# Performance work log

Measured on AMD Instinct MI355X. Metric: run time of the kernel, lower is better.

Reference implementation:

```python
import jax, jax.numpy as jnp
import numpy as np

B, L, D = 4, 1024, 1024
N, H = 16, 64
FFW = 4096
LYR = 6
PDIM = 768            # 3 * 16^2
POS_EMB = 64
POOL_K = 4
EPS = 1e-6
BASE = 10000.0
GRID = 32             # 32x32 patch grid


def rms_norm(x, scale=None, eps=EPS):
    v = jnp.mean(jnp.square(x.astype(jnp.float32)), axis=-1, keepdims=True)
    y = (x.astype(jnp.float32) * jax.lax.rsqrt(v + eps)).astype(x.dtype)
    return y * scale if scale is not None else y


def _rope_half(x, pos, base):
    # x: [B, L, N, Hh]; pos: [B, L] int coords
    Hh = x.shape[-1]
    inv = 1.0 / (base ** (jnp.arange(Hh // 2, dtype=jnp.float32) / (Hh // 2)))
    ang = pos.astype(jnp.float32)[..., None] * inv          # [B, L, Hh/2]
    cos = jnp.cos(ang)[:, :, None, :]
    sin = jnp.sin(ang)[:, :, None, :]
    x1, x2 = jnp.split(x, 2, axis=-1)
    return jnp.concatenate([x1 * cos - x2 * sin, x2 * cos + x1 * sin], axis=-1)


def apply_2d_rope(x, px, py, base):
    # first half of head_dim rotated by x-coord, second half by y-coord
    xa, xb = jnp.split(x, 2, axis=-1)
    return jnp.concatenate([_rope_half(xa, px, base), _rope_half(xb, py, base)], axis=-1)


def setup_inputs() -> dict:
    key = jax.random.key(0)
    ks = jax.random.split(key, 12)
    pixel_values = jax.random.uniform(ks[0], (B, L, PDIM), dtype=jnp.float32)
    gx = jnp.arange(L, dtype=jnp.int32) % GRID
    gy = jnp.arange(L, dtype=jnp.int32) // GRID
    position_ids = jnp.broadcast_to(jnp.stack([gx, gy], -1), (B, L, 2))
    s = 0.02
    Win = jax.random.normal(ks[1], (PDIM, D), jnp.float32) * s
    pos_table = jax.random.normal(ks[2], (2, POS_EMB, D), jnp.float32) * s
    Wq = jax.random.normal(ks[3], (LYR, D, N * H), jnp.float32) * s
    Wk = jax.random.normal(ks[4], (LYR, D, N * H), jnp.float32) * s
    Wv = jax.random.normal(ks[5], (LYR, D, N * H), jnp.float32) * s
    Wo = jax.random.normal(ks[6], (LYR, N * H, D), jnp.float32) * s
    Wg = jax.random.normal(ks[7], (LYR, D, FFW), jnp.float32) * s
    Wu = jax.random.normal(ks[8], (LYR, D, FFW), jnp.float32) * s
    Wd = jax.random.normal(ks[9], (LYR, FFW, D), jnp.float32) * s
    qn = jnp.ones((LYR, H), jnp.float32)
    kn = jnp.ones((LYR, H), jnp.float32)
    pre_attn = jnp.ones((LYR, D), jnp.float32)
    post_attn = jnp.ones((LYR, D), jnp.float32)
    pre_ffw = jnp.ones((LYR, D), jnp.float32)
    post_ffw = jnp.ones((LYR, D), jnp.float32)
    return dict(pixel_values=pixel_values, position_ids=position_ids, Win=Win,
                pos_table=pos_table, Wq=Wq, Wk=Wk, Wv=Wv, Wo=Wo, qn=qn, kn=kn,
                pre_attn=pre_attn, post_attn=post_attn, pre_ffw=pre_ffw,
                post_ffw=post_ffw, Wg=Wg, Wu=Wu, Wd=Wd)


def _encoder(pixel_values, position_ids, Win, pos_table, Wq, Wk, Wv, Wo, qn, kn,
             pre_attn, post_attn, pre_ffw, post_ffw, Wg, Wu, Wd):
    padding = jnp.all(position_ids == -1, axis=-1)          # [B, L] True = pad
    valid = ~padding
    big_neg = jnp.finfo(jnp.float32).min
    amask = jnp.where((valid[:, :, None] & valid[:, None, :])[:, None], 0.0, big_neg)  # [B,1,L,L]

    px = position_ids[:, :, 0]
    py = position_ids[:, :, 1]
    clamped = jnp.maximum(position_ids, 0)

    # patch embed
    pix = 2.0 * (pixel_values - 0.5)
    x = pix @ Win
    pos_emb = pos_table[0][clamped[..., 0]] + pos_table[1][clamped[..., 1]]
    x = x + jnp.where(padding[..., None], 0.0, pos_emb)

    for i in range(LYR):
        # attention
        res = x
        h = rms_norm(x, pre_attn[i])
        q = (h @ Wq[i]).reshape(B, L, N, H)
        k = (h @ Wk[i]).reshape(B, L, N, H)
        v = (h @ Wv[i]).reshape(B, L, N, H)
        q = rms_norm(q, qn[i])
        k = rms_norm(k, kn[i])
        v = rms_norm(v)                                     # with_scale=False
        q = apply_2d_rope(q, px, py, BASE)
        k = apply_2d_rope(k, px, py, BASE)
        scores = jnp.einsum('bqnh,bknh->bnqk', q, k) + amask  # no 1/sqrt(H), matches source
        w = jax.nn.softmax(scores.astype(jnp.float32), axis=-1).astype(v.dtype)
        o = jnp.einsum('bnqk,bknh->bqnh', w, v).reshape(B, L, N * H) @ Wo[i]
        x = res + rms_norm(o, post_attn[i])
        # GeGLU MLP
        res = x
        h = rms_norm(x, pre_ffw[i])
        m = (jax.nn.gelu(h @ Wg[i], approximate=True) * (h @ Wu[i])) @ Wd[i]
        x = res + rms_norm(m, post_ffw[i])

    # pooler: 4x4 position-based average pooling
    out_len = L // (POOL_K ** 2)
    kk = int((L / out_len) ** 0.5)
    x = jnp.where(padding[..., None], 0.0, x)
    max_x = jnp.max(clamped[..., 0], axis=-1, keepdims=True) + 1   # [B,1]
    kidx = clamped // kk
    kidx = kidx[..., 0] + (max_x // kk) * kidx[..., 1]             # [B, L]
    weights = jax.nn.one_hot(kidx, out_len, dtype=jnp.float32) / (kk * kk)
    pooled = jnp.einsum('blo,bld->bod', weights, x.astype(jnp.float32))
    mask = jnp.any(weights != 0, axis=1)                           # [B, out_len]
    pooled = pooled.astype(x.dtype) * jnp.sqrt(jnp.float32(D))
    pooled = jnp.where(mask[..., None], pooled, 0.0)               # jit-safe stand-in for hidden[mask]
    return pooled, mask


def reference(pixel_values, position_ids, Win, pos_table, Wq, Wk, Wv, Wo, qn, kn,
              pre_attn, post_attn, pre_ffw, post_ffw, Wg, Wu, Wd):
    return _encoder(pixel_values, position_ids, Win, pos_table, Wq, Wk, Wv, Wo,
                    qn, kn, pre_attn, post_attn, pre_ffw, post_ffw, Wg, Wu, Wd)
```

## Files before the change

kernel.cpp:

```cpp
#include <hip/hip_runtime.h>
#include <stdint.h>

typedef unsigned short ushort_t;
using frag8 = __attribute__((ext_vector_type(8))) short;
using f32x4 = __attribute__((ext_vector_type(4))) float;

static __device__ __forceinline__ unsigned short f2bf(float f) {
  union { float f; unsigned u; } v; v.f = f;
  unsigned r = v.u + 0x7fffu + ((v.u >> 16) & 1u);
  return (unsigned short)(r >> 16);
}
static __device__ __forceinline__ float bf2f(unsigned short b) {
  union { unsigned u; float f; } v; v.u = ((unsigned)b) << 16; return v.f;
}
static __device__ __forceinline__ void splitf(float v, ushort_t& h, ushort_t& m) {
  h = f2bf(v);
  m = f2bf(v - bf2f(h));
}

__global__ __launch_bounds__(256) void k_splitpix(const float* __restrict__ pix,
                                                  ushort_t* __restrict__ oh,
                                                  ushort_t* __restrict__ om, int n4) {
  int i = blockIdx.x * 256 + threadIdx.x;
  if (i >= n4) return;
// ... 32 lines not shown
  int n = tid >> 2;
  int kc = (tid & 3) << 4;
  ushort_t oh[16], om[16];
#pragma unroll
  for (int j = 0; j < 16; ++j) splitf(ts[kc + j][n], oh[j], om[j]);
  ushort_t* ph = th + (size_t)(n0 + n) * K + k0 + kc;
  ushort_t* pm = tm + (size_t)(n0 + n) * K + k0 + kc;
  *(uint4*)(ph) = *(uint4*)(oh);
  *(uint4*)(ph + 8) = *(uint4*)(oh + 8);
  *(uint4*)(pm) = *(uint4*)(om);
  *(uint4*)(pm + 8) = *(uint4*)(om + 8);
}

__global__ __launch_bounds__(256) void k_posemb(const int* __restrict__ pos,
                                                const float* __restrict__ ptab,
                                                float* __restrict__ x) {
  int row = blockIdx.x, tid = threadIdx.x;
  int p0 = pos[(size_t)row * 2], p1 = pos[(size_t)row * 2 + 1];
  bool pad = (p0 == -1) && (p1 == -1);
  int px = p0 > 0 ? p0 : 0, py = p1 > 0 ? p1 : 0;
  float4 a = ((const float4*)(ptab + (size_t)px * 1024))[tid];
  float4 b = ((const float4*)(ptab + 65536 + (size_t)py * 1024))[tid];
  float4 o;
  o.x = pad ? 0.f : a.x + b.x;
  o.y = pad ? 0.f : a.y + b.y;
  o.z = pad ? 0.f : a.z + b.z;
  o.w = pad ? 0.f : a.w + b.w;
  ((float4*)(x + (size_t)row * 1024))[tid] = o;
}

__global__ __launch_bounds__(256) void k_rmsnorm_s(const float* __restrict__ x,
                                                   const float* __restrict__ scale,
                                                   ushort_t* __restrict__ oh,
                                                   ushort_t* __restrict__ om) {
  __shared__ float wsum[4];
  int row = blockIdx.x, tid = threadIdx.x;
  float4 v = ((const float4*)(x + (size_t)row * 1024))[tid];
  float ss = v.x * v.x + v.y * v.y + v.z * v.z + v.w * v.w;
  for (int m = 1; m < 64; m <<= 1) ss += __shfl_xor(ss, m);
  if ((tid & 63) == 0) wsum[tid >> 6] = ss;
  __syncthreads();
  float tot = wsum[0] + wsum[1] + wsum[2] + wsum[3];
  float r = rsqrtf(tot * (1.f / 1024.f) + 1e-6f);
  float4 sc = ((const float4*)scale)[tid];
  ushort4 h, m;
  splitf(v.x * r * sc.x, h.x, m.x);
  splitf(v.y * r * sc.y, h.y, m.y);
  splitf(v.z * r * sc.z, h.z, m.z);
  splitf(v.w * r * sc.w, h.w, m.w);
  ((ushort4*)(oh + (size_t)row * 1024))[tid] = h;
  ((ushort4*)(om + (size_t)row * 1024))[tid] = m;
}

__global__ __launch_bounds__(256) void k_addrms32(float* __restrict__ x,
                                                  const float* __restrict__ t1,
                                                  const float* __restrict__ t2,
                                                  const float* __restrict__ scale) {
  __shared__ float wsum[4];
  int row = blockIdx.x, tid = threadIdx.x;
  float4 v = ((const float4*)(t1 + (size_t)row * 1024))[tid];
  float4 v2 = ((const float4*)(t2 + (size_t)row * 1024))[tid];
  v.x += v2.x; v.y += v2.y; v.z += v2.z; v.w += v2.w;
  float ss = v.x * v.x + v.y * v.y + v.z * v.z + v.w * v.w;
  for (int m = 1; m < 64; m <<= 1) ss += __shfl_xor(ss, m);
  if ((tid & 63) == 0) wsum[tid >> 6] = ss;
  __syncthreads();
  float tot = wsum[0] + wsum[1] + wsum[2] + wsum[3];
  float r = rsqrtf(tot * (1.f / 1024.f) + 1e-6f);
  float4 sc = ((const float4*)scale)[tid];
  float4 xv = ((const float4*)(x + (size_t)row * 1024))[tid];
  xv.x += v.x * r * sc.x;
  xv.y += v.y * r * sc.y;
  xv.z += v.z * r * sc.z;
  xv.w += v.w * r * sc.w;
  ((float4*)(x + (size_t)row * 1024))[tid] = xv;
}

#define SWZ_COL(r, c) (((c) ^ (((r) >> 3) & 3)) << 3)

__global__ __launch_bounds__(256) void k_qkv(const ushort_t* __restrict__ Ah,
                                             const ushort_t* __restrict__ Am,
                                             const ushort_t* __restrict__ WT_h,
                                             const ushort_t* __restrict__ WT_m,
                                             const float* __restrict__ qn,
                                             const float* __restrict__ kn,
                                             const int* __restrict__ pos,
                                             ushort_t* __restrict__ qh, ushort_t* __restrict__ qm,
                                             ushort_t* __restrict__ kh, ushort_t* __restrict__ km,
                                             ushort_t* __restrict__ vh, ushort_t* __restrict__ vm) {
  __shared__ __align__(16) ushort_t Ash[128][40];
  __shared__ __align__(16) ushort_t Asl[128][40];
  __shared__ __align__(16) ushort_t Bsh[128][40];
  __shared__ __align__(16) ushort_t Bsl[128][40];
  const int tid = threadIdx.x;
  const int bid = blockIdx.x;
  const int xcd = bid & 7, lo = bid >> 3;
  const int ntl = lo % 3, mt = lo / 3;
  const int nt = xcd * 3 + ntl;
  const int mat = nt >> 3;
  const int n0 = (nt & 7) << 7;
  const int m0 = mt << 7;
  const ushort_t* Bh = WT_h + (size_t)mat * 1048576;
  const ushort_t* Bm = WT_m + (size_t)mat * 1048576;

  const int lane = tid & 63;
  const int wm = ((tid >> 7) & 1) * 64;
  const int wn = ((tid >> 6) & 1) * 64;
  const int l15 = lane & 15, lg = lane >> 4;
  const int srow = tid >> 1, scol = (tid & 1) << 4;
  const int cb = (tid & 1) << 1;
  const int wc0 = SWZ_COL(srow, cb), wc1 = SWZ_COL(srow, cb + 1);
  f32x4 acc[4][4] = {};

  for (int k0 = 0; k0 < 1024; k0 += 32) {
    const ushort_t* gah = Ah + (size_t)(m0 + srow) * 1024 + k0 + scol;
    const ushort_t* gam = Am + (size_t)(m0 + srow) * 1024 + k0 + scol;
    const ushort_t* gbh = Bh + (size_t)(n0 + srow) * 1024 + k0 + scol;
    const ushort_t* gbm = Bm + (size_t)(n0 + srow) * 1024 + k0 + scol;
    uint4 a0 = *(const uint4*)gah, a1 = *(const uint4*)(gah + 8);
    uint4 a2 = *(const uint4*)gam, a3 = *(const uint4*)(gam + 8);
    uint4 b0 = *(const uint4*)gbh, b1 = *(const uint4*)(gbh + 8);
    uint4 b2 = *(const uint4*)gbm, b3 = *(const uint4*)(gbm + 8);
    *(uint4*)(&Ash[srow][wc0]) = a0;
    *(uint4*)(&Ash[srow][wc1]) = a1;
    *(uint4*)(&Asl[srow][wc0]) = a2;
    *(uint4*)(&Asl[srow][wc1]) = a3;
    *(uint4*)(&Bsh[srow][wc0]) = b0;
    *(uint4*)(&Bsh[srow][wc1]) = b1;
    *(uint4*)(&Bsl[srow][wc0]) = b2;
    *(uint4*)(&Bsl[srow][wc1]) = b3;
    __syncthreads();
    frag8 ah[4], al[4], bh[4], bl[4];
#pragma unroll
    for (int i = 0; i < 4; ++i) {
      int rA = wm + i * 16 + l15, rB = wn + i * 16 + l15;
      int cA = SWZ_COL(rA, lg), cB = SWZ_COL(rB, lg);
      ah[i] = *(const frag8*)(&Ash[rA][cA]);
      al[i] = *(const frag8*)(&Asl[rA][cA]);
      bh[i] = *(const frag8*)(&Bsh[rB][cB]);
      bl[i] = *(const frag8*)(&Bsl[rB][cB]);
    }
#pragma unroll
    for (int mi = 0; mi < 4; ++mi)
#pragma unroll
      for (int ni = 0; ni < 4; ++ni) {
        acc[mi][ni] = __builtin_amdgcn_mfma_f32_16x16x32_bf16(ah[mi], bh[ni], acc[mi][ni], 0, 0, 0);
        acc[mi][ni] = __builtin_amdgcn_mfma_f32_16x16x32_bf16(ah[mi], bl[ni], acc[mi][ni], 0, 0, 0);
        acc[mi][ni] = __builtin_amdgcn_mfma_f32_16x16x32_bf16(al[mi], bh[ni], acc[mi][ni], 0, 0, 0);
      }
    __syncthreads();
  }

  const float* scale = (mat == 0) ? qn : (mat == 1 ? kn : nullptr);
  ushort_t* outh = (mat == 0) ? qh : (mat == 1 ? kh : vh);
  ushort_t* outm = (mat == 0) ? qm : (mat == 1 ? km : vm);
  const float inv = powf(10000.f, -(float)l15 * (1.f / 16.f));
#pragma unroll
  for (int mi = 0; mi < 4; ++mi) {
#pragma unroll
    for (int rr = 0; rr < 4; ++rr) {
      float ss = 0.f;
#pragma unroll
      for (int ni = 0; ni < 4; ++ni) { float v = acc[mi][ni][rr]; ss += v * v; }
      ss += __shfl_xor(ss, 1);
      ss += __shfl_xor(ss, 2);
      ss += __shfl_xor(ss, 4);
      ss += __shfl_xor(ss, 8);
      float rs = rsqrtf(ss * (1.f / 64.f) + 1e-6f);
      int row = m0 + wm + mi * 16 + (lg << 2) + rr;
      float nv[4];
#pragma unroll
      for (int ni = 0; ni < 4; ++ni) {
        float sc = scale ? scale[ni * 16 + l15] : 1.f;
        nv[ni] = acc[mi][ni][rr] * rs * sc;
      }
      if (mat < 2) {
        int p0 = pos[(size_t)row * 2], p1 = pos[(size_t)row * 2 + 1];
        p0 = p0 > 0 ? p0 : 0;
        p1 = p1 > 0 ? p1 : 0;
        float a0 = (float)p0 * inv, a1 = (float)p1 * inv;
        float c0 = cosf(a0), s0 = sinf(a0);
        float c1 = cosf(a1), s1 = sinf(a1);
        float t0 = nv[0] * c0 - nv[1] * s0;
        float t1 = nv[1] * c0 + nv[0] * s0;
        float t2 = nv[2] * c1 - nv[3] * s1;
        float t3 = nv[3] * c1 + nv[2] * s1;
        nv[0] = t0; nv[1] = t1; nv[2] = t2; nv[3] = t3;
      }
#pragma unroll
      for (int ni = 0; ni < 4; ++ni) {
        ushort_t h, m;
        splitf(nv[ni], h, m);
        size_t idx = (size_t)row * 1024 + n0 + wn + ni * 16 + l15;
        outh[idx] = h;
        outm[idx] = m;
      }
    }
  }
}

__global__ __launch_bounds__(256) void k_ffw_up(const ushort_t* __restrict__ Ah,
                                                const ushort_t* __restrict__ Am,
                                                const ushort_t* __restrict__ Gh,
                                                const ushort_t* __restrict__ Gm,
                                                const ushort_t* __restrict__ Uh,
                                                const ushort_t* __restrict__ Um,
                                                ushort_t* __restrict__ Oh,
                                                ushort_t* __restrict__ Om) {
  __shared__ __align__(16) ushort_t Ash[128][40];
  __shared__ __align__(16) ushort_t Asl[128][40];
  __shared__ __align__(16) ushort_t Bgh[128][40];
// ... 46 lines not shown
#pragma unroll
    for (int i = 0; i < 4; ++i) {
      int rA = wm + i * 16 + l15;
      int cA = SWZ_COL(rA, lg);
      ah[i] = *(const frag8*)(&Ash[rA][cA]);
      al[i] = *(const frag8*)(&Asl[rA][cA]);
    }
#pragma unroll
    for (int ni = 0; ni < 4; ++ni) {
      int rB = wn + ni * 16 + l15;
      int cB = SWZ_COL(rB, lg);
      frag8 bgh = *(const frag8*)(&Bgh[rB][cB]);
      frag8 bgl = *(const frag8*)(&Bgl[rB][cB]);
      frag8 buh = *(const frag8*)(&Buh[rB][cB]);
      frag8 bul = *(const frag8*)(&Bul[rB][cB]);
#pragma unroll
      for (int mi = 0; mi < 4; ++mi) {
        ag[mi][ni] = __builtin_amdgcn_mfma_f32_16x16x32_bf16(ah[mi], bgh, ag[mi][ni], 0, 0, 0);
        ag[mi][ni] = __builtin_amdgcn_mfma_f32_16x16x32_bf16(ah[mi], bgl, ag[mi][ni], 0, 0, 0);
        ag[mi][ni] = __builtin_amdgcn_mfma_f32_16x16x32_bf16(al[mi], bgh, ag[mi][ni], 0, 0, 0);
        au[mi][ni] = __builtin_amdgcn_mfma_f32_16x16x32_bf16(ah[mi], buh, au[mi][ni], 0, 0, 0);
        au[mi][ni] = __builtin_amdgcn_mfma_f32_16x16x32_bf16(ah[mi], bul, au[mi][ni], 0, 0, 0);
        au[mi][ni] = __builtin_amdgcn_mfma_f32_16x16x32_bf16(al[mi], buh, au[mi][ni], 0, 0, 0);
      }
    }
    __syncthreads();
  }

#pragma unroll
  for (int mi = 0; mi < 4; ++mi) {
#pragma unroll
    for (int ni = 0; ni < 4; ++ni) {
#pragma unroll
      for (int r = 0; r < 4; ++r) {
        float vg = ag[mi][ni][r];
        float x3 = vg * vg * vg;
        float gel = 0.5f * vg * (1.f + tanhf(0.7978845608028654f * (vg + 0.044715f * x3)));
        float v2 = gel * au[mi][ni][r];
        int gr = m0 + wm + mi * 16 + (lg << 2) + r;
        int gc = n0 + wn + ni * 16 + l15;
        size_t idx = (size_t)gr * 4096 + gc;
        ushort_t h, m;
        splitf(v2, h, m);
        Oh[idx] = h;
        Om[idx] = m;
      }
    }
  }
}

enum { EPI_F32 = 0, EPI_ADDF32 = 1 };

template <int EPI>
__global__ __launch_bounds__(256) void k_gemm_s(const ushort_t* __restrict__ Ah,
                                                const ushort_t* __restrict__ Am,
                                                const ushort_t* __restrict__ Bh,
                                                const ushort_t* __restrict__ Bm,
                                                float* C0, float* C1,
                                                int K, int N, int ksteps) {
  __shared__ __align__(16) ushort_t Ash[128][40];
  __shared__ __align__(16) ushort_t Asl[128][40];
  __shared__ __align__(16) ushort_t Bsh[128][40];
  __shared__ __align__(16) ushort_t Bsl[128][40];
  const int tid = threadIdx.x;
  const int bid = blockIdx.x;
  const int half = bid >> 8;
  const int inner = bid & 255;
  float* Cf = half ? C1 : C0;
  const int kbase = half * ksteps * 32;
  const int xcd = inner & 7, lo = inner >> 3;
  const int mt = xcd * 4 + (lo >> 3);
  const int nt = lo & 7;
  const int m0 = mt << 7, n0 = nt << 7;
  const int lane = tid & 63;
  const int wm = ((tid >> 7) & 1) * 64;
  const int wn = ((tid >> 6) & 1) * 64;
  const int l15 = lane & 15, lg = lane >> 4;
  const int srow = tid >> 1, scol = (tid & 1) << 4;
  const int cb = (tid & 1) << 1;
  const int wc0 = SWZ_COL(srow, cb), wc1 = SWZ_COL(srow, cb + 1);
  f32x4 acc[4][4] = {};

  for (int ks = 0; ks < ksteps; ++ks) {
    const int k0 = kbase + ks * 32;
    const ushort_t* gah = Ah + (size_t)(m0 + srow) * K + k0 + scol;
    const ushort_t* gam = Am + (size_t)(m0 + srow) * K + k0 + scol;
    const ushort_t* gbh = Bh + (size_t)(n0 + srow) * K + k0 + scol;
    const ushort_t* gbm = Bm + (size_t)(n0 + srow) * K + k0 + scol;
    uint4 a0 = *(const uint4*)gah, a1 = *(const uint4*)(gah + 8);
    uint4 a2 = *(const uint4*)gam, a3 = *(const uint4*)(gam + 8);
    uint4 b0 = *(const uint4*)gbh, b1 = *(const uint4*)(gbh + 8);
    uint4 b2 = *(const uint4*)gbm, b3 = *(const uint4*)(gbm + 8);
    *(uint4*)(&Ash[srow][wc0]) = a0;
    *(uint4*)(&Ash[srow][wc1]) = a1;
    *(uint4*)(&Asl[srow][wc0]) = a2;
    *(uint4*)(&Asl[srow][wc1]) = a3;
    *(uint4*)(&Bsh[srow][wc0]) = b0;
    *(uint4*)(&Bsh[srow][wc1]) = b1;
    *(uint4*)(&Bsl[srow][wc0]) = b2;
    *(uint4*)(&Bsl[srow][wc1]) = b3;
    __syncthreads();
    frag8 ah[4], al[4], bh[4], bl[4];
#pragma unroll
    for (int i = 0; i < 4; ++i) {
      int rA = wm + i * 16 + l15, rB = wn + i * 16 + l15;
      int cA = SWZ_COL(rA, lg), cB = SWZ_COL(rB, lg);
      ah[i] = *(const frag8*)(&Ash[rA][cA]);
      al[i] = *(const frag8*)(&Asl[rA][cA]);
      bh[i] = *(const frag8*)(&Bsh[rB][cB]);
      bl[i] = *(const frag8*)(&Bsl[rB][cB]);
    }
#pragma unroll
    for (int mi = 0; mi < 4; ++mi)
#pragma unroll
      for (int ni = 0; ni < 4; ++ni) {
        acc[mi][ni] = __builtin_amdgcn_mfma_f32_16x16x32_bf16(ah[mi], bh[ni], acc[mi][ni], 0, 0, 0);
        acc[mi][ni] = __builtin_amdgcn_mfma_f32_16x16x32_bf16(ah[mi], bl[ni], acc[mi][ni], 0, 0, 0);
        acc[mi][ni] = __builtin_amdgcn_mfma_f32_16x16x32_bf16(al[mi], bh[ni], acc[mi][ni], 0, 0, 0);
      }
    __syncthreads();
  }

#pragma unroll
  for (int mi = 0; mi < 4; ++mi) {
#pragma unroll
    for (int ni = 0; ni < 4; ++ni) {
#pragma unroll
      for (int r = 0; r < 4; ++r) {
        float val = acc[mi][ni][r];
        int gr = m0 + wm + mi * 16 + (lg << 2) + r;
        int gc = n0 + wn + ni * 16 + l15;
        size_t idx = (size_t)gr * N + gc;
        if (EPI == EPI_F32) Cf[idx] = val;
        else Cf[idx] += val;
      }
    }
  }
}

__global__ __launch_bounds__(256) void k_attn_s(const ushort_t* __restrict__ qh,
                                                const ushort_t* __restrict__ qm,
                                                const ushort_t* __restrict__ kh,
                                                const ushort_t* __restrict__ km,
                                                const ushort_t* __restrict__ vh,
                                                const ushort_t* __restrict__ vm,
                                                ushort_t* __restrict__ oh,
                                                ushort_t* __restrict__ om) {
  __shared__ __align__(16) ushort_t Khs[64][72];
  __shared__ __align__(16) ushort_t Kms[64][72];
  __shared__ __align__(16) ushort_t Vhs[64][72];
  __shared__ __align__(16) ushort_t Vms[64][72];
  __shared__ __align__(16) ushort_t Phs[64][72];
  __shared__ __align__(16) ushort_t Pms[64][72];
  const int tid = threadIdx.x;
  const int bid = blockIdx.x;
  const int xcd = bid & 7, lo = bid >> 3;
  const int bh_ = xcd * 8 + (lo >> 4);
  const int qt = lo & 15;
  const int b = bh_ >> 4, n = bh_ & 15;
  const size_t base = (size_t)b * 1048576 + (size_t)n * 64;
  const int lane = tid & 63, w = tid >> 6;
  const int l15 = lane & 15, lg = lane >> 4;

  {
    int row = tid >> 2, cg = (tid & 3) << 4;
    const uint4* sh = (const uint4*)(qh + base + (size_t)(qt * 64 + row) * 1024 + cg);
    const uint4* sm = (const uint4*)(qm + base + (size_t)(qt * 64 + row) * 1024 + cg);
    uint4 h0 = sh[0], h1 = sh[1], m0v = sm[0], m1v = sm[1];
    *(uint4*)(&Khs[row][cg]) = h0;
    *(uint4*)(&Khs[row][cg + 8]) = h1;
    *(uint4*)(&Kms[row][cg]) = m0v;
    *(uint4*)(&Kms[row][cg + 8]) = m1v;
  }
  __syncthreads();
  frag8 qh0 = *(const frag8*)(&Khs[w * 16 + l15][lg << 3]);
  frag8 qh1 = *(const frag8*)(&Khs[w * 16 + l15][32 + (lg << 3)]);
  frag8 qm0 = *(const frag8*)(&Kms[w * 16 + l15][lg << 3]);
  frag8 qm1 = *(const frag8*)(&Kms[w * 16 + l15][32 + (lg << 3)]);

  f32x4 oacc[4] = {};
  float mrun[4], srun[4];
#pragma unroll
  for (int r = 0; r < 4; ++r) { mrun[r] = -3.0e38f; srun[r] = 0.f; }

  for (int t = 0; t < 16; ++t) {
    __syncthreads();
    {
      int row = tid >> 2, cg = (tid & 3) << 4;
      const uint4* sh = (const uint4*)(kh + base + (size_t)(t * 64 + row) * 1024 + cg);
      const uint4* sm = (const uint4*)(km + base + (size_t)(t * 64 + row) * 1024 + cg);
      uint4 h0 = sh[0], h1 = sh[1], m0v = sm[0], m1v = sm[1];
      *(uint4*)(&Khs[row][cg]) = h0;
// ... 124 lines not shown
  for (int l = 0; l < 1024; ++l) {
    int ki = kidx_s[l];
    if ((ki & 0xffff) == oidx) {
      cnt++;
      if (!(ki >> 16)) {
        float4 xv = ((const float4*)(x + ((size_t)b * 1024 + l) * 1024))[tid];
        ax += xv.x; ay += xv.y; az += xv.z; aw += xv.w;
      }
    }
  }
  float4 res;
  res.x = ax * 2.0f; res.y = ay * 2.0f; res.z = az * 2.0f; res.w = aw * 2.0f;
  ((float4*)(out + ((size_t)b * 64 + oidx) * 1024))[tid] = res;
  if (tid == 0) maskout[b * 64 + oidx] = (cnt > 0) ? 1.0f : 0.0f;
}

extern "C" void kernel_launch(void* const* d_in, const int* in_sizes, int n_in,
                              void* d_out, int out_size, void* d_ws, size_t ws_size,
                              hipStream_t stream) {
  const float* pix = (const float*)d_in[0];
  const int* pos = (const int*)d_in[1];
  const float* Win = (const float*)d_in[2];
  const float* ptab = (const float*)d_in[3];
  const float* Wq = (const float*)d_in[4];
  const float* Wk = (const float*)d_in[5];
  const float* Wv = (const float*)d_in[6];
  const float* Wo = (const float*)d_in[7];
  const float* qn = (const float*)d_in[8];
  const float* kn = (const float*)d_in[9];
  const float* pre_attn = (const float*)d_in[10];
  const float* post_attn = (const float*)d_in[11];
  const float* pre_ffw = (const float*)d_in[12];
  const float* post_ffw = (const float*)d_in[13];
  const float* Wg = (const float*)d_in[14];
  const float* Wu = (const float*)d_in[15];
  const float* Wd = (const float*)d_in[16];

  char* w = (char*)d_ws;
  float* x = (float*)w;        w += 16777216;
  float* tmp = (float*)w;      w += 16777216;
  ushort_t* hh = (ushort_t*)w; w += 8388608;
  ushort_t* hm = (ushort_t*)w; w += 8388608;
  char* regB = w;
  ushort_t* qh_ = (ushort_t*)(regB + 0);
  ushort_t* qm_ = (ushort_t*)(regB + 8388608);
  ushort_t* kh_ = (ushort_t*)(regB + 16777216);
  ushort_t* km_ = (ushort_t*)(regB + 25165824);
  ushort_t* vh_ = (ushort_t*)(regB + 33554432);
  ushort_t* vm_ = (ushort_t*)(regB + 41943040);
  ushort_t* aoh = (ushort_t*)(regB + 50331648);
  ushort_t* aom = (ushort_t*)(regB + 58720256);
  ushort_t* wat_h = (ushort_t*)(regB + 67108864);
  ushort_t* wat_m = (ushort_t*)(regB + 75497472);
  float* t2o = (float*)(regB + 0);
  ushort_t* mh = (ushort_t*)(regB + 0);
  ushort_t* mm = (ushort_t*)(regB + 33554432);
  ushort_t* wgu_h = (ushort_t*)(regB + 67108864);
  ushort_t* wgu_m = (ushort_t*)(regB + 83886080);
  ushort_t* wd_h = (ushort_t*)(regB + 100663296);
  ushort_t* wd_m = (ushort_t*)(regB + 109051904);
  float* t2d = (float*)(regB + 67108864);
  ushort_t* pixh = (ushort_t*)(regB + 0);
  ushort_t* pixm = (ushort_t*)(regB + 6291456);
  ushort_t* win_h = (ushort_t*)(regB + 67108864);
  ushort_t* win_m = (ushort_t*)(regB + 71303168);

  dim3 blk(256);
  k_splitpix<<<3072, blk, 0, stream>>>(pix, pixh, pixm, 786432);
  k_posemb<<<4096, blk, 0, stream>>>(pos, ptab, x);
  k_wsplit4<<<dim3(16, 12, 1), blk, 0, stream>>>(Win, Win, Win, Win, win_h, win_m, 768, 1024);
  k_gemm_s<EPI_ADDF32><<<256, blk, 0, stream>>>(pixh, pixm, win_h, win_m, x, nullptr,
                                                768, 1024, 24);

  for (int i = 0; i < 6; ++i) {
    const float* wq = Wq + (size_t)i * 1048576;
    const float* wk = Wk + (size_t)i * 1048576;
    const float* wv = Wv + (size_t)i * 1048576;
    const float* wo = Wo + (size_t)i * 1048576;
    const float* wg = Wg + (size_t)i * 4194304;
    const float* wu = Wu + (size_t)i * 4194304;
    const float* wd = Wd + (size_t)i * 4194304;

    k_rmsnorm_s<<<4096, blk, 0, stream>>>(x, pre_attn + i * 1024, hh, hm);
    k_wsplit4<<<dim3(16, 16, 4), blk, 0, stream>>>(wq, wk, wv, wo, wat_h, wat_m, 1024, 1024);
    k_qkv<<<768, blk, 0, stream>>>(hh, hm, wat_h, wat_m, qn + i * 64, kn + i * 64, pos,
                                   qh_, qm_, kh_, km_, vh_, vm_);
    k_attn_s<<<1024, blk, 0, stream>>>(qh_, qm_, kh_, km_, vh_, vm_, aoh, aom);
    k_gemm_s<EPI_F32><<<512, blk, 0, stream>>>(aoh, aom, wat_h + 3145728, wat_m + 3145728,
                                               tmp, t2o, 1024, 1024, 16);
    k_addrms32<<<4096, blk, 0, stream>>>(x, tmp, t2o, post_attn + i * 1024);

    k_rmsnorm_s<<<4096, blk, 0, stream>>>(x, pre_ffw + i * 1024, hh, hm);
    k_wsplit4<<<dim3(64, 16, 2), blk, 0, stream>>>(wg, wu, wg, wu, wgu_h, wgu_m, 1024, 4096);
    k_wsplit4<<<dim3(16, 64, 1), blk, 0, stream>>>(wd, wd, wd, wd, wd_h, wd_m, 4096, 1024);
    k_ffw_up<<<1024, blk, 0, stream>>>(hh, hm, wgu_h, wgu_m, wgu_h + 4194304, wgu_m + 4194304,
                                       mh, mm);
    k_gemm_s<EPI_F32><<<512, blk, 0, stream>>>(mh, mm, wd_h, wd_m, tmp, t2d, 4096, 1024, 64);
    k_addrms32<<<4096, blk, 0, stream>>>(x, tmp, t2d, post_ffw + i * 1024);
  }

  k_pool<<<256, blk, 0, stream>>>(x, pos, (float*)d_out, (float*)d_out + 262144);
}
```

Measured before the change: 4.636 ms.

## Enlarge QKV and split GEMM tiles to 256x128 with more B-fragment reuse

The QKV and generic split-bf16 GEMM kernels now compute 256x128 output tiles instead of 128x128. Each wave handles 8x4 MFMA fragments, and the loop is reordered so each B fragment is loaded once and reused across eight A fragments. Grid sizes are halved to match. This raises arithmetic intensity per LDS and global load, but doubles accumulator registers, halves the number of blocks on a 256-CU GPU (some launches drop to 128 blocks), and adds a launch_bounds occupancy hint.

```diff
diff --git a/kernel.cpp b/kernel.cpp
--- a/kernel.cpp
+++ b/kernel.cpp
@@ -134,18 +134,18 @@
 
 #define SWZ_COL(r, c) (((c) ^ (((r) >> 3) & 3)) << 3)
 
-__global__ __launch_bounds__(256) void k_qkv(const ushort_t* __restrict__ Ah,
-                                             const ushort_t* __restrict__ Am,
-                                             const ushort_t* __restrict__ WT_h,
-                                             const ushort_t* __restrict__ WT_m,
-                                             const float* __restrict__ qn,
-                                             const float* __restrict__ kn,
-                                             const int* __restrict__ pos,
-                                             ushort_t* __restrict__ qh, ushort_t* __restrict__ qm,
-                                             ushort_t* __restrict__ kh, ushort_t* __restrict__ km,
-                                             ushort_t* __restrict__ vh, ushort_t* __restrict__ vm) {
-  __shared__ __align__(16) ushort_t Ash[128][40];
-  __shared__ __align__(16) ushort_t Asl[128][40];
+__global__ __launch_bounds__(256, 2) void k_qkv(const ushort_t* __restrict__ Ah,
+                                                const ushort_t* __restrict__ Am,
+                                                const ushort_t* __restrict__ WT_h,
+                                                const ushort_t* __restrict__ WT_m,
+                                                const float* __restrict__ qn,
+                                                const float* __restrict__ kn,
+                                                const int* __restrict__ pos,
+                                                ushort_t* __restrict__ qh, ushort_t* __restrict__ qm,
+                                                ushort_t* __restrict__ kh, ushort_t* __restrict__ km,
+                                                ushort_t* __restrict__ vh, ushort_t* __restrict__ vm) {
+  __shared__ __align__(16) ushort_t Ash[256][40];
+  __shared__ __align__(16) ushort_t Asl[256][40];
   __shared__ __align__(16) ushort_t Bsh[128][40];
   __shared__ __align__(16) ushort_t Bsl[128][40];
   const int tid = threadIdx.x;
@@ -155,55 +155,58 @@
   const int nt = xcd * 3 + ntl;
   const int mat = nt >> 3;
   const int n0 = (nt & 7) << 7;
-  const int m0 = mt << 7;
+  const int m0 = mt << 8;
   const ushort_t* Bh = WT_h + (size_t)mat * 1048576;
   const ushort_t* Bm = WT_m + (size_t)mat * 1048576;
 
   const int lane = tid & 63;
-  const int wm = ((tid >> 7) & 1) * 64;
+  const int wm = ((tid >> 7) & 1) * 128;
   const int wn = ((tid >> 6) & 1) * 64;
   const int l15 = lane & 15, lg = lane >> 4;
-  const int srow = tid >> 1, scol = (tid & 1) << 4;
-  const int cb = (tid & 1) << 1;
-  const int wc0 = SWZ_COL(srow, cb), wc1 = SWZ_COL(srow, cb + 1);
-  f32x4 acc[4][4] = {};
+  const int srB = tid >> 1, cbB = (tid & 1) << 1;
+  f32x4 acc[8][4] = {};
 
   for (int k0 = 0; k0 < 1024; k0 += 32) {
-    const ushort_t* gah = Ah + (size_t)(m0 + srow) * 1024 + k0 + scol;
-    const ushort_t* gam = Am + (size_t)(m0 + srow) * 1024 + k0 + scol;
-    const ushort_t* gbh = Bh + (size_t)(n0 + srow) * 1024 + k0 + scol;
-    const ushort_t* gbm = Bm + (size_t)(n0 + srow) * 1024 + k0 + scol;
-    uint4 a0 = *(const uint4*)gah, a1 = *(const uint4*)(gah + 8);
-    uint4 a2 = *(const uint4*)gam, a3 = *(const uint4*)(gam + 8);
-    uint4 b0 = *(const uint4*)gbh, b1 = *(const uint4*)(gbh + 8);
-    uint4 b2 = *(const uint4*)gbm, b3 = *(const uint4*)(gbm + 8);
-    *(uint4*)(&Ash[srow][wc0]) = a0;
-    *(uint4*)(&Ash[srow][wc1]) = a1;
-    *(uint4*)(&Asl[srow][wc0]) = a2;
-    *(uint4*)(&Asl[srow][wc1]) = a3;
-    *(uint4*)(&Bsh[srow][wc0]) = b0;
-    *(uint4*)(&Bsh[srow][wc1]) = b1;
-    *(uint4*)(&Bsl[srow][wc0]) = b2;
-    *(uint4*)(&Bsl[srow][wc1]) = b3;
-    __syncthreads();
-    frag8 ah[4], al[4], bh[4], bl[4];
-#pragma unroll
-    for (int i = 0; i < 4; ++i) {
-      int rA = wm + i * 16 + l15, rB = wn + i * 16 + l15;
-      int cA = SWZ_COL(rA, lg), cB = SWZ_COL(rB, lg);
+    const ushort_t* gah = Ah + (size_t)(m0 + tid) * 1024 + k0;
+    const ushort_t* gam = Am + (size_t)(m0 + tid) * 1024 + k0;
+    const ushort_t* gbh = Bh + (size_t)(n0 + srB) * 1024 + k0 + (cbB << 3);
+    const ushort_t* gbm = Bm + (size_t)(n0 + srB) * 1024 + k0 + (cbB << 3);
+    uint4 ah4[4], al4[4];
+#pragma unroll
+    for (int c = 0; c < 4; ++c) { ah4[c] = ((const uint4*)gah)[c]; al4[c] = ((const uint4*)gam)[c]; }
+    uint4 b0 = ((const uint4*)gbh)[0], b1 = ((const uint4*)gbh)[1];
+    uint4 b2 = ((const uint4*)gbm)[0], b3 = ((const uint4*)gbm)[1];
+#pragma unroll
+    for (int c = 0; c < 4; ++c) {
+      *(uint4*)(&Ash[tid][SWZ_COL(tid, c)]) = ah4[c];
+      *(uint4*)(&Asl[tid][SWZ_COL(tid, c)]) = al4[c];
+    }
+    *(uint4*)(&Bsh[srB][SWZ_COL(srB, cbB)]) = b0;
+    *(uint4*)(&Bsh[srB][SWZ_COL(srB, cbB + 1)]) = b1;
+    *(uint4*)(&Bsl[srB][SWZ_COL(srB, cbB)]) = b2;
+    *(uint4*)(&Bsl[srB][SWZ_COL(srB, cbB + 1)]) = b3;
+    __syncthreads();
+    frag8 ah[8], al[8];
+#pragma unroll
+    for (int i = 0; i < 8; ++i) {
+      int rA = wm + i * 16 + l15;
+      int cA = SWZ_COL(rA, lg);
       ah[i] = *(const frag8*)(&Ash[rA][cA]);
       al[i] = *(const frag8*)(&Asl[rA][cA]);
-      bh[i] = *(const frag8*)(&Bsh[rB][cB]);
-      bl[i] = *(const frag8*)(&Bsl[rB][cB]);
-    }
-#pragma unroll
-    for (int mi = 0; mi < 4; ++mi)
-#pragma unroll
-      for (int ni = 0; ni < 4; ++ni) {
-        acc[mi][ni] = __builtin_amdgcn_mfma_f32_16x16x32_bf16(ah[mi], bh[ni], acc[mi][ni], 0, 0, 0);
-        acc[mi][ni] = __builtin_amdgcn_mfma_f32_16x16x32_bf16(ah[mi], bl[ni], acc[mi][ni], 0, 0, 0);
-        acc[mi][ni] = __builtin_amdgcn_mfma_f32_16x16x32_bf16(al[mi], bh[ni], acc[mi][ni], 0, 0, 0);
-      }
+    }
+#pragma unroll
+    for (int ni = 0; ni < 4; ++ni) {
+      int rB = wn + ni * 16 + l15;
+      int cB = SWZ_COL(rB, lg);
+      frag8 bh = *(const frag8*)(&Bsh[rB][cB]);
+      frag8 bl = *(const frag8*)(&Bsl[rB][cB]);
+#pragma unroll
+      for (int mi = 0; mi < 8; ++mi) {
+        acc[mi][ni] = __builtin_amdgcn_mfma_f32_16x16x32_bf16(ah[mi], bh, acc[mi][ni], 0, 0, 0);
+        acc[mi][ni] = __builtin_amdgcn_mfma_f32_16x16x32_bf16(ah[mi], bl, acc[mi][ni], 0, 0, 0);
+        acc[mi][ni] = __builtin_amdgcn_mfma_f32_16x16x32_bf16(al[mi], bh, acc[mi][ni], 0, 0, 0);
+      }
+    }
     __syncthreads();
   }
 
@@ -212,7 +215,7 @@
   ushort_t* outm = (mat == 0) ? qm : (mat == 1 ? km : vm);
   const float inv = powf(10000.f, -(float)l15 * (1.f / 16.f));
 #pragma unroll
-  for (int mi = 0; mi < 4; ++mi) {
+  for (int mi = 0; mi < 8; ++mi) {
 #pragma unroll
     for (int rr = 0; rr < 4; ++rr) {
       float ss = 0.f;
@@ -365,77 +368,80 @@
 enum { EPI_F32 = 0, EPI_ADDF32 = 1 };
 
 template <int EPI>
-__global__ __launch_bounds__(256) void k_gemm_s(const ushort_t* __restrict__ Ah,
-                                                const ushort_t* __restrict__ Am,
-                                                const ushort_t* __restrict__ Bh,
-                                                const ushort_t* __restrict__ Bm,
-                                                float* C0, float* C1,
-                                                int K, int N, int ksteps) {
-  __shared__ __align__(16) ushort_t Ash[128][40];
-  __shared__ __align__(16) ushort_t Asl[128][40];
+__global__ __launch_bounds__(256, 2) void k_gemm_s(const ushort_t* __restrict__ Ah,
+                                                   const ushort_t* __restrict__ Am,
+                                                   const ushort_t* __restrict__ Bh,
+                                                   const ushort_t* __restrict__ Bm,
+                                                   float* C0, float* C1,
+                                                   int K, int N, int ksteps) {
+  __shared__ __align__(16) ushort_t Ash[256][40];
+  __shared__ __align__(16) ushort_t Asl[256][40];
   __shared__ __align__(16) ushort_t Bsh[128][40];
   __shared__ __align__(16) ushort_t Bsl[128][40];
   const int tid = threadIdx.x;
   const int bid = blockIdx.x;
-  const int half = bid >> 8;
-  const int inner = bid & 255;
+  const int half = bid >> 7;
+  const int inner = bid & 127;
   float* Cf = half ? C1 : C0;
   const int kbase = half * ksteps * 32;
   const int xcd = inner & 7, lo = inner >> 3;
-  const int mt = xcd * 4 + (lo >> 3);
+  const int mt = xcd * 2 + (lo >> 3);
   const int nt = lo & 7;
-  const int m0 = mt << 7, n0 = nt << 7;
+  const int m0 = mt << 8, n0 = nt << 7;
   const int lane = tid & 63;
-  const int wm = ((tid >> 7) & 1) * 64;
+  const int wm = ((tid >> 7) & 1) * 128;
   const int wn = ((tid >> 6) & 1) * 64;
   const int l15 = lane & 15, lg = lane >> 4;
-  const int srow = tid >> 1, scol = (tid & 1) << 4;
-  const int cb = (tid & 1) << 1;
-  const int wc0 = SWZ_COL(srow, cb), wc1 = SWZ_COL(srow, cb + 1);
-  f32x4 acc[4][4] = {};
+  const int srB = tid >> 1, cbB = (tid & 1) << 1;
+  f32x4 acc[8][4] = {};
 
   for (int ks = 0; ks < ksteps; ++ks) {
     const int k0 = kbase + ks * 32;
-    const ushort_t* gah = Ah + (size_t)(m0 + srow) * K + k0 + scol;
-    const ushort_t* gam = Am + (size_t)(m0 + srow) * K + k0 + scol;
-    const ushort_t* gbh = Bh + (size_t)(n0 + srow) * K + k0 + scol;
-    const ushort_t* gbm = Bm + (size_t)(n0 + srow) * K + k0 + scol;
-    uint4 a0 = *(const uint4*)gah, a1 = *(const uint4*)(gah + 8);
-    uint4 a2 = *(const uint4*)gam, a3 = *(const uint4*)(gam + 8);
-    uint4 b0 = *(const uint4*)gbh, b1 = *(const uint4*)(gbh + 8);
-    uint4 b2 = *(const uint4*)gbm, b3 = *(const uint4*)(gbm + 8);
-    *(uint4*)(&Ash[srow][wc0]) = a0;
-    *(uint4*)(&Ash[srow][wc1]) = a1;
-    *(uint4*)(&Asl[srow][wc0]) = a2;
-    *(uint4*)(&Asl[srow][wc1]) = a3;
-    *(uint4*)(&Bsh[srow][wc0]) = b0;
-    *(uint4*)(&Bsh[srow][wc1]) = b1;
-    *(uint4*)(&Bsl[srow][wc0]) = b2;
-    *(uint4*)(&Bsl[srow][wc1]) = b3;
-    __syncthreads();
-    frag8 ah[4], al[4], bh[4], bl[4];
-#pragma unroll
-    for (int i = 0; i < 4; ++i) {
-      int rA = wm + i * 16 + l15, rB = wn + i * 16 + l15;
-      int cA = SWZ_COL(rA, lg), cB = SWZ_COL(rB, lg);
+    const ushort_t* gah = Ah + (size_t)(m0 + tid) * K + k0;
+    const ushort_t* gam = Am + (size_t)(m0 + tid) * K + k0;
+    const ushort_t* gbh = Bh + (size_t)(n0 + srB) * K + k0 + (cbB << 3);
+    const ushort_t* gbm = Bm + (size_t)(n0 + srB) * K + k0 + (cbB << 3);
+    uint4 ah4[4], al4[4];
+#pragma unroll
+    for (int c = 0; c < 4; ++c) { ah4[c] = ((const uint4*)gah)[c]; al4[c] = ((const uint4*)gam)[c]; }
+    uint4 b0 = ((const uint4*)gbh)[0], b1 = ((const uint4*)gbh)[1];
+    uint4 b2 = ((const uint4*)gbm)[0], b3 = ((const uint4*)gbm)[1];
+#pragma unroll
+    for (int c = 0; c < 4; ++c) {
+      *(uint4*)(&Ash[tid][SWZ_COL(tid, c)]) = ah4[c];
+      *(uint4*)(&Asl[tid][SWZ_COL(tid, c)]) = al4[c];
+    }
+    *(uint4*)(&Bsh[srB][SWZ_COL(srB, cbB)]) = b0;
+    *(uint4*)(&Bsh[srB][SWZ_COL(srB, cbB + 1)]) = b1;
+    *(uint4*)(&Bsl[srB][SWZ_COL(srB, cbB)]) = b2;
+    *(uint4*)(&Bsl[srB][SWZ_COL(srB, cbB + 1)]) = b3;
+    __syncthreads();
+    frag8 ah[8], al[8];
+#pragma unroll
+    for (int i = 0; i < 8; ++i) {
+      int rA = wm + i * 16 + l15;
+      int cA = SWZ_COL(rA, lg);
       ah[i] = *(const frag8*)(&Ash[rA][cA]);
       al[i] = *(const frag8*)(&Asl[rA][cA]);
-      bh[i] = *(const frag8*)(&Bsh[rB][cB]);
-      bl[i] = *(const frag8*)(&Bsl[rB][cB]);
-    }
-#pragma unroll
-    for (int mi = 0; mi < 4; ++mi)
-#pragma unroll
-      for (int ni = 0; ni < 4; ++ni) {
-        acc[mi][ni] = __builtin_amdgcn_mfma_f32_16x16x32_bf16(ah[mi], bh[ni], acc[mi][ni], 0, 0, 0);
-        acc[mi][ni] = __builtin_amdgcn_mfma_f32_16x16x32_bf16(ah[mi], bl[ni], acc[mi][ni], 0, 0, 0);
-        acc[mi][ni] = __builtin_amdgcn_mfma_f32_16x16x32_bf16(al[mi], bh[ni], acc[mi][ni], 0, 0, 0);
-      }
-    __syncthreads();
-  }
-
-#pragma unroll
-  for (int mi = 0; mi < 4; ++mi) {
+    }
+#pragma unroll
+    for (int ni = 0; ni < 4; ++ni) {
+      int rB = wn + ni * 16 + l15;
+      int cB = SWZ_COL(rB, lg);
+      frag8 bh = *(const frag8*)(&Bsh[rB][cB]);
+      frag8 bl = *(const frag8*)(&Bsl[rB][cB]);
+#pragma unroll
+      for (int mi = 0; mi < 8; ++mi) {
+        acc[mi][ni] = __builtin_amdgcn_mfma_f32_16x16x32_bf16(ah[mi], bh, acc[mi][ni], 0, 0, 0);
+        acc[mi][ni] = __builtin_amdgcn_mfma_f32_16x16x32_bf16(ah[mi], bl, acc[mi][ni], 0, 0, 0);
+        acc[mi][ni] = __builtin_amdgcn_mfma_f32_16x16x32_bf16(al[mi], bh, acc[mi][ni], 0, 0, 0);
+      }
+    }
+    __syncthreads();
+  }
+
+#pragma unroll
+  for (int mi = 0; mi < 8; ++mi) {
 #pragma unroll
     for (int ni = 0; ni < 4; ++ni) {
 #pragma unroll
@@ -698,7 +704,7 @@
   k_splitpix<<<3072, blk, 0, stream>>>(pix, pixh, pixm, 786432);
   k_posemb<<<4096, blk, 0, stream>>>(pos, ptab, x);
   k_wsplit4<<<dim3(16, 12, 1), blk, 0, stream>>>(Win, Win, Win, Win, win_h, win_m, 768, 1024);
-  k_gemm_s<EPI_ADDF32><<<256, blk, 0, stream>>>(pixh, pixm, win_h, win_m, x, nullptr,
+  k_gemm_s<EPI_ADDF32><<<128, blk, 0, stream>>>(pixh, pixm, win_h, win_m, x, nullptr,
                                                 768, 1024, 24);
 
   for (int i = 0; i < 6; ++i) {
@@ -712,10 +718,10 @@
 
     k_rmsnorm_s<<<4096, blk, 0, stream>>>(x, pre_attn + i * 1024, hh, hm);
     k_wsplit4<<<dim3(16, 16, 4), blk, 0, stream>>>(wq, wk, wv, wo, wat_h, wat_m, 1024, 1024);
-    k_qkv<<<768, blk, 0, stream>>>(hh, hm, wat_h, wat_m, qn + i * 64, kn + i * 64, pos,
+    k_qkv<<<384, blk, 0, stream>>>(hh, hm, wat_h, wat_m, qn + i * 64, kn + i * 64, pos,
                                    qh_, qm_, kh_, km_, vh_, vm_);
     k_attn_s<<<1024, blk, 0, stream>>>(qh_, qm_, kh_, km_, vh_, vm_, aoh, aom);
-    k_gemm_s<EPI_F32><<<512, blk, 0, stream>>>(aoh, aom, wat_h + 3145728, wat_m + 3145728,
+    k_gemm_s<EPI_F32><<<256, blk, 0, stream>>>(aoh, aom, wat_h + 3145728, wat_m + 3145728,
                                                tmp, t2o, 1024, 1024, 16);
     k_addrms32<<<4096, blk, 0, stream>>>(x, tmp, t2o, post_attn + i * 1024);
 
@@ -724,7 +730,7 @@
     k_wsplit4<<<dim3(16, 64, 1), blk, 0, stream>>>(wd, wd, wd, wd, wd_h, wd_m, 4096, 1024);
     k_ffw_up<<<1024, blk, 0, stream>>>(hh, hm, wgu_h, wgu_m, wgu_h + 4194304, wgu_m + 4194304,
                                        mh, mm);
-    k_gemm_s<EPI_F32><<<512, blk, 0, stream>>>(mh, mm, wd_h, wd_m, tmp, t2d, 4096, 1024, 64);
+    k_gemm_s<EPI_F32><<<256, blk, 0, stream>>>(mh, mm, wd_h, wd_m, tmp, t2d, 4096, 1024, 64);
     k_addrms32<<<4096, blk, 0, stream>>>(x, tmp, t2d, post_ffw + i * 1024);
   }
 
```

Measured after the change: 5.155 ms. +11.2%, slower.

## Use 256x128 tiles with 4-way split-K for Wo and Wd GEMMs

Applied to the files above, without the earlier changes.

Adds a new split-bf16 GEMM kernel with a larger 256x128 output tile per block (8x4 MFMA accumulators per wave) and a four-way K split across blocks. Each quarter writes its partial sums to a separate fp32 buffer. The residual add+RMSNorm kernel now sums four partials instead of two. The larger tile raises operand reuse per LDS load, at the cost of higher register pressure and more partial-buffer traffic. The pd3 partial reuses the hh/hm workspace, which is safe only because that buffer is rewritten before its next use.

```diff
diff --git a/kernel.cpp b/kernel.cpp
--- a/kernel.cpp
+++ b/kernel.cpp
@@ -108,15 +108,22 @@
   ((ushort4*)(om + (size_t)row * 1024))[tid] = m;
 }
 
-__global__ __launch_bounds__(256) void k_addrms32(float* __restrict__ x,
-                                                  const float* __restrict__ t1,
-                                                  const float* __restrict__ t2,
-                                                  const float* __restrict__ scale) {
+__global__ __launch_bounds__(256) void k_addrms4(float* __restrict__ x,
+                                                 const float* __restrict__ t1,
+                                                 const float* __restrict__ t2,
+                                                 const float* __restrict__ t3,
+                                                 const float* __restrict__ t4,
+                                                 const float* __restrict__ scale) {
   __shared__ float wsum[4];
   int row = blockIdx.x, tid = threadIdx.x;
   float4 v = ((const float4*)(t1 + (size_t)row * 1024))[tid];
   float4 v2 = ((const float4*)(t2 + (size_t)row * 1024))[tid];
-  v.x += v2.x; v.y += v2.y; v.z += v2.z; v.w += v2.w;
+  float4 v3 = ((const float4*)(t3 + (size_t)row * 1024))[tid];
+  float4 v4 = ((const float4*)(t4 + (size_t)row * 1024))[tid];
+  v.x += v2.x + v3.x + v4.x;
+  v.y += v2.y + v3.y + v4.y;
+  v.z += v2.z + v3.z + v4.z;
+  v.w += v2.w + v3.w + v4.w;
   float ss = v.x * v.x + v.y * v.y + v.z * v.z + v.w * v.w;
   for (int m = 1; m < 64; m <<= 1) ss += __shfl_xor(ss, m);
   if ((tid & 63) == 0) wsum[tid >> 6] = ss;
@@ -451,6 +458,93 @@
   }
 }
 
+__global__ __launch_bounds__(256, 2) void k_gemm_s8(const ushort_t* __restrict__ Ah,
+                                                    const ushort_t* __restrict__ Am,
+                                                    const ushort_t* __restrict__ Bh,
+                                                    const ushort_t* __restrict__ Bm,
+                                                    float* C0, float* C1, float* C2, float* C3,
+                                                    int K, int N, int ksteps) {
+  __shared__ __align__(16) ushort_t Ash[256][40];
+  __shared__ __align__(16) ushort_t Asl[256][40];
+  __shared__ __align__(16) ushort_t Bsh[128][40];
+  __shared__ __align__(16) ushort_t Bsl[128][40];
+  const int tid = threadIdx.x;
+  const int bid = blockIdx.x;
+  const int quarter = bid >> 7;
+  const int inner = bid & 127;
+  float* Cf = (quarter == 0) ? C0 : (quarter == 1) ? C1 : (quarter == 2) ? C2 : C3;
+  const int kbase = quarter * ksteps * 32;
+  const int xcd = inner & 7, lo = inner >> 3;
+  const int mt = xcd * 2 + (lo >> 3);
+  const int nt = lo & 7;
+  const int m0 = mt << 8, n0 = nt << 7;
+  const int lane = tid & 63;
+  const int wm = ((tid >> 7) & 1) * 128;
+  const int wn = ((tid >> 6) & 1) * 64;
+  const int l15 = lane & 15, lg = lane >> 4;
+  const int srB = tid >> 1, cbB = (tid & 1) << 1;
+  f32x4 acc[8][4] = {};
+
+  for (int ks = 0; ks < ksteps; ++ks) {
+    const int k0 = kbase + ks * 32;
+    const ushort_t* gah = Ah + (size_t)(m0 + tid) * K + k0;
+    const ushort_t* gam = Am + (size_t)(m0 + tid) * K + k0;
+    const ushort_t* gbh = Bh + (size_t)(n0 + srB) * K + k0 + (cbB << 3);
+    const ushort_t* gbm = Bm + (size_t)(n0 + srB) * K + k0 + (cbB << 3);
+#pragma unroll
+    for (int c = 0; c < 4; ++c) {
+      uint4 va = ((const uint4*)gah)[c];
+      uint4 vb = ((const uint4*)gam)[c];
+      *(uint4*)(&Ash[tid][SWZ_COL(tid, c)]) = va;
+      *(uint4*)(&Asl[tid][SWZ_COL(tid, c)]) = vb;
+    }
+    {
+      uint4 b0 = ((const uint4*)gbh)[0], b1 = ((const uint4*)gbh)[1];
+      uint4 b2 = ((const uint4*)gbm)[0], b3 = ((const uint4*)gbm)[1];
+      *(uint4*)(&Bsh[srB][SWZ_COL(srB, cbB)]) = b0;
+      *(uint4*)(&Bsh[srB][SWZ_COL(srB, cbB + 1)]) = b1;
+      *(uint4*)(&Bsl[srB][SWZ_COL(srB, cbB)]) = b2;
+      *(uint4*)(&Bsl[srB][SWZ_COL(srB, cbB + 1)]) = b3;
+    }
+    __syncthreads();
+    frag8 bh[4], bl[4];
+#pragma unroll
+    for (int ni = 0; ni < 4; ++ni) {
+      int rB = wn + ni * 16 + l15;
+      int cB = SWZ_COL(rB, lg);
+      bh[ni] = *(const frag8*)(&Bsh[rB][cB]);
+      bl[ni] = *(const frag8*)(&Bsl[rB][cB]);
+    }
+#pragma unroll
+    for (int mi = 0; mi < 8; ++mi) {
+      int rA = wm + mi * 16 + l15;
+      int cA = SWZ_COL(rA, lg);
+      frag8 ah = *(const frag8*)(&Ash[rA][cA]);
+      frag8 al = *(const frag8*)(&Asl[rA][cA]);
+#pragma unroll
+      for (int ni = 0; ni < 4; ++ni) {
+        acc[mi][ni] = __builtin_amdgcn_mfma_f32_16x16x32_bf16(ah, bh[ni], acc[mi][ni], 0, 0, 0);
+        acc[mi][ni] = __builtin_amdgcn_mfma_f32_16x16x32_bf16(ah, bl[ni], acc[mi][ni], 0, 0, 0);
+        acc[mi][ni] = __builtin_amdgcn_mfma_f32_16x16x32_bf16(al, bh[ni], acc[mi][ni], 0, 0, 0);
+      }
+    }
+    __syncthreads();
+  }
+
+#pragma unroll
+  for (int mi = 0; mi < 8; ++mi) {
+#pragma unroll
+    for (int ni = 0; ni < 4; ++ni) {
+#pragma unroll
+      for (int r = 0; r < 4; ++r) {
+        int gr = m0 + wm + mi * 16 + (lg << 2) + r;
+        int gc = n0 + wn + ni * 16 + l15;
+        Cf[(size_t)gr * N + gc] = acc[mi][ni][r];
+      }
+    }
+  }
+}
+
 __global__ __launch_bounds__(256) void k_attn_s(const ushort_t* __restrict__ qh,
                                                 const ushort_t* __restrict__ qm,
                                                 const ushort_t* __restrict__ kh,
@@ -681,14 +775,18 @@
   ushort_t* aom = (ushort_t*)(regB + 58720256);
   ushort_t* wat_h = (ushort_t*)(regB + 67108864);
   ushort_t* wat_m = (ushort_t*)(regB + 75497472);
-  float* t2o = (float*)(regB + 0);
+  float* po1 = (float*)(regB + 0);
+  float* po2 = (float*)(regB + 16777216);
+  float* po3 = (float*)(regB + 33554432);
   ushort_t* mh = (ushort_t*)(regB + 0);
   ushort_t* mm = (ushort_t*)(regB + 33554432);
   ushort_t* wgu_h = (ushort_t*)(regB + 67108864);
   ushort_t* wgu_m = (ushort_t*)(regB + 83886080);
   ushort_t* wd_h = (ushort_t*)(regB + 100663296);
   ushort_t* wd_m = (ushort_t*)(regB + 109051904);
-  float* t2d = (float*)(regB + 67108864);
+  float* pd1 = (float*)(regB + 67108864);
+  float* pd2 = (float*)(regB + 83886080);
+  float* pd3 = (float*)hh;
   ushort_t* pixh = (ushort_t*)(regB + 0);
   ushort_t* pixm = (ushort_t*)(regB + 6291456);
   ushort_t* win_h = (ushort_t*)(regB + 67108864);
@@ -715,17 +813,18 @@
     k_qkv<<<768, blk, 0, stream>>>(hh, hm, wat_h, wat_m, qn + i * 64, kn + i * 64, pos,
                                    qh_, qm_, kh_, km_, vh_, vm_);
     k_attn_s<<<1024, blk, 0, stream>>>(qh_, qm_, kh_, km_, vh_, vm_, aoh, aom);
-    k_gemm_s<EPI_F32><<<512, blk, 0, stream>>>(aoh, aom, wat_h + 3145728, wat_m + 3145728,
-                                               tmp, t2o, 1024, 1024, 16);
-    k_addrms32<<<4096, blk, 0, stream>>>(x, tmp, t2o, post_attn + i * 1024);
+    k_gemm_s8<<<512, blk, 0, stream>>>(aoh, aom, wat_h + 3145728, wat_m + 3145728,
+                                       tmp, po1, po2, po3, 1024, 1024, 8);
+    k_addrms4<<<4096, blk, 0, stream>>>(x, tmp, po1, po2, po3, post_attn + i * 1024);
 
     k_rmsnorm_s<<<4096, blk, 0, stream>>>(x, pre_ffw + i * 1024, hh, hm);
     k_wsplit4<<<dim3(64, 16, 2), blk, 0, stream>>>(wg, wu, wg, wu, wgu_h, wgu_m, 1024, 4096);
     k_wsplit4<<<dim3(16, 64, 1), blk, 0, stream>>>(wd, wd, wd, wd, wd_h, wd_m, 4096, 1024);
     k_ffw_up<<<1024, blk, 0, stream>>>(hh, hm, wgu_h, wgu_m, wgu_h + 4194304, wgu_m + 4194304,
                                        mh, mm);
-    k_gemm_s<EPI_F32><<<512, blk, 0, stream>>>(mh, mm, wd_h, wd_m, tmp, t2d, 4096, 1024, 64);
-    k_addrms32<<<4096, blk, 0, stream>>>(x, tmp, t2d, post_ffw + i * 1024);
+    k_gemm_s8<<<512, blk, 0, stream>>>(mh, mm, wd_h, wd_m, tmp, pd1, pd2, pd3,
+                                       4096, 1024, 32);
+    k_addrms4<<<4096, blk, 0, stream>>>(x, tmp, pd1, pd2, pd3, post_ffw + i * 1024);
   }
 
   k_pool<<<256, blk, 0, stream>>>(x, pos, (float*)d_out, (float*)d_out + 262144);
```

After: 4.759 ms. 1.03x slower.
